# Optimization experiments

Hardware: AMD Instinct MI355X
Metric: run time of the kernel (lower is better)

The kernel has to match this reference:

```python
import jax, jax.numpy as jnp
import numpy as np

STEP_SIZE = 0.01
ITERATION = 1.0
F_FORCING = 8.0
N_STEPS = int(round(ITERATION / STEP_SIZE))  # 100 fixed RK4 steps

BATCH = 8192
INPUT_SIZE = 784
SYSTEM_COUNT = 1024
OUTPUT_SIZE = 10


def setup_inputs() -> dict:
    key = jax.random.key(0)
    k_x, k_w1, k_b1, k_w2, k_b2 = jax.random.split(key, 5)
    x = jax.random.normal(k_x, (BATCH, INPUT_SIZE), dtype=jnp.float32)
    # nn.Linear-style params (out_features, in_features)
    s1 = 1.0 / np.sqrt(INPUT_SIZE)
    W1 = jax.random.uniform(k_w1, (SYSTEM_COUNT, INPUT_SIZE), jnp.float32, -s1, s1)
    b1 = jax.random.uniform(k_b1, (SYSTEM_COUNT,), jnp.float32, -s1, s1)
    s2 = 1.0 / np.sqrt(SYSTEM_COUNT)
    W2 = jax.random.uniform(k_w2, (OUTPUT_SIZE, SYSTEM_COUNT), jnp.float32, -s2, s2)
    b2 = jax.random.uniform(k_b2, (OUTPUT_SIZE,), jnp.float32, -s2, s2)
    return {"x": x, "W1": W1, "b1": b1, "W2": W2, "b2": b2}


def _lorenz96(x):
    # (roll(x,-1) - roll(x,2)) * roll(x,1) - x + F   along feature dim 1
    return (jnp.roll(x, -1, axis=1) - jnp.roll(x, 2, axis=1)) * jnp.roll(x, 1, axis=1) - x + F_FORCING


def _rk4_integrate(x0):
    h = jnp.float32(STEP_SIZE)

    def step(x, _):
        k1 = _lorenz96(x)
        k2 = _lorenz96(x + 0.5 * h * k1)
        k3 = _lorenz96(x + 0.5 * h * k2)
        k4 = _lorenz96(x + h * k3)
        x_next = x + (h / 6.0) * (k1 + 2.0 * k2 + 2.0 * k3 + k4)
        return x_next, None

    xT, _ = jax.lax.scan(step, x0, None, length=N_STEPS)
    return xT


def reference(x, W1, b1, W2, b2):
    h = x @ W1.T + b1                 # [B, systemCount]
    h = _rk4_integrate(h)             # RK4 over [0, iteration], step 0.01
    logits = h @ W2.T + b2            # [B, output_size]
    return jax.nn.log_softmax(logits, axis=1)
```

## Files before the change

### kernel.cpp

```cpp
#include <hip/hip_runtime.h>
#include <hip/hip_bf16.h>
#include <math.h>

#define BATCH 8192
#define INSZ 784
#define SYS 1024
#define OUTSZ 10
#define NSTEP 100
#define HSTEP 0.01f
#define FFORCE 8.0f
#define KP 800

typedef short short8 __attribute__((ext_vector_type(8)));
typedef float float4v __attribute__((ext_vector_type(4)));
typedef float v2f __attribute__((ext_vector_type(2)));

static __device__ __forceinline__ short f2bf(float x) {
    __hip_bfloat16 b = __float2bfloat16(x);
    return __builtin_bit_cast(short, b);
}
static __device__ __forceinline__ float bf2f(short s) {
    unsigned int u = ((unsigned int)(unsigned short)s) << 16;
    return __builtin_bit_cast(float, u);
}

static __device__ __forceinline__ v2f pkfma(v2f a, v2f b, v2f c) {
    return __builtin_elementwise_fma(a, b, c);
}
static __device__ __forceinline__ v2f mk2(float x, float y) {
    v2f r; r.x = x; r.y = y; return r;
}
static __device__ __forceinline__ v2f sh2(v2f v, int ln) {
    v2f r; r.x = __shfl(v.x, ln); r.y = __shfl(v.y, ln); return r;
}

static __device__ __forceinline__ void gld_lds16(const void* g, void* l) {
    __builtin_amdgcn_global_load_lds(
        (const __attribute__((address_space(1))) unsigned int*)g,
        (__attribute__((address_space(3))) unsigned int*)l, 16, 0, 0);
}

__global__ __launch_bounds__(256) void convert_kernel(
    const float* __restrict__ x, const float* __restrict__ W1,
    short* __restrict__ xh, short* __restrict__ xl,
    short* __restrict__ wh, short* __restrict__ wl)
{
    const int total = (BATCH + SYS) * (KP / 8);
    for (int idx = blockIdx.x * blockDim.x + threadIdx.x; idx < total;
         idx += gridDim.x * blockDim.x) {
        const int row = idx / (KP / 8);
        const int ck  = idx - row * (KP / 8);

        short8 hi, lo;
        if (ck < INSZ / 8) {
            const float* src = (row < BATCH)
                ? (x + (size_t)row * INSZ)
                : (W1 + (size_t)(row - BATCH) * INSZ);
            float4 v0 = ((const float4*)src)[ck * 2];
            float4 v1 = ((const float4*)src)[ck * 2 + 1];
            float vv[8] = {v0.x, v0.y, v0.z, v0.w, v1.x, v1.y, v1.z, v1.w};
            #pragma unroll
            for (int j = 0; j < 8; ++j) {
                short hj = f2bf(vv[j]);
                hi[j] = hj;
                lo[j] = f2bf(vv[j] - bf2f(hj));
            }
        } else {
            #pragma unroll
            for (int j = 0; j < 8; ++j) { hi[j] = 0; lo[j] = 0; }
        }

        short* dh; short* dl;
        if (row < BATCH) {
            dh = xh + (size_t)row * KP;
            dl = xl + (size_t)row * KP;
        } else {
            dh = wh + (size_t)(row - BATCH) * KP;
            dl = wl + (size_t)(row - BATCH) * KP;
        }
        *(short8*)(dh + ck * 8) = hi;
        *(short8*)(dl + ck * 8) = lo;
    }
}

#define BM4 128
#define BN4 256
#define BK4 32

__global__ __launch_bounds__(512, 4) void gemm1s_kernel(
    const short* __restrict__ xh, const short* __restrict__ xl,
    const short* __restrict__ wh, const short* __restrict__ wl,
    const float* __restrict__ b1, float* __restrict__ h)
{
    __shared__ short Ah[BM4 * BK4], Al[BM4 * BK4];
    __shared__ short Bh[BN4 * BK4], Bl[BN4 * BK4];

    const int t = threadIdx.x;

    const int lin = blockIdx.y * gridDim.x + blockIdx.x;
    const int cpx = (gridDim.x * gridDim.y) >> 3;
    const int swz = (lin & 7) * cpx + (lin >> 3);
    const int bm  = (swz >> 2) * BM4;
    const int bn  = (swz & 3) * BN4;

    const int wv   = t >> 6;
    const int lane = t & 63;
    const int lm   = lane & 15;
    const int q    = lane >> 4;
    const int wr   = wv >> 2;
    const int wc   = wv & 3;

    float4v acc[4][4];
    #pragma unroll
    for (int mi = 0; mi < 4; ++mi)
        #pragma unroll
        for (int nj = 0; nj < 4; ++nj) {
            acc[mi][nj][0] = 0.f; acc[mi][nj][1] = 0.f;
            acc[mi][nj][2] = 0.f; acc[mi][nj][3] = 0.f;
        }

    const int srA = wv * 16 + (lane >> 2);
    const int kqq = (lane & 3) * 8;
    const short* gAh = xh + (size_t)(bm + srA) * KP + kqq;
    const short* gAl = xl + (size_t)(bm + srA) * KP + kqq;
    const short* gB0h = wh + (size_t)(bn + srA) * KP + kqq;
    const short* gB0l = wl + (size_t)(bn + srA) * KP + kqq;
    const short* gB1h = wh + (size_t)(bn + 128 + srA) * KP + kqq;
    const short* gB1l = wl + (size_t)(bn + 128 + srA) * KP + kqq;

    short* lAh = &Ah[wv * 512];
    short* lAl = &Al[wv * 512];
    short* lB0h = &Bh[wv * 512];
    short* lB0l = &Bl[wv * 512];
    short* lB1h = &Bh[4096 + wv * 512];
    short* lB1l = &Bl[4096 + wv * 512];

    gld_lds16(gAh, lAh);   gld_lds16(gAl, lAl);
    gld_lds16(gB0h, lB0h); gld_lds16(gB0l, lB0l);
    gld_lds16(gB1h, lB1h); gld_lds16(gB1l, lB1l);

    for (int it = 0; it < 25; ++it) {
        __syncthreads();

        short8 fah[4], fal[4];
        #pragma unroll
        for (int mi = 0; mi < 4; ++mi) {
            const int ao = (wr * 64 + mi * 16 + lm) * BK4 + q * 8;
            fah[mi] = *(const short8*)&Ah[ao];
            fal[mi] = *(const short8*)&Al[ao];
        }
        short8 fbh[4], fbl[4];
        #pragma unroll
        for (int nj = 0; nj < 4; ++nj) {
            const int bo = (wc * 64 + nj * 16 + lm) * BK4 + q * 8;
            fbh[nj] = *(const short8*)&Bh[bo];
            fbl[nj] = *(const short8*)&Bl[bo];
        }
        __syncthreads();

        if (it < 24) {
            const int k1 = (it + 1) * BK4;
            gld_lds16(gAh + k1, lAh);   gld_lds16(gAl + k1, lAl);
            gld_lds16(gB0h + k1, lB0h); gld_lds16(gB0l + k1, lB0l);
            gld_lds16(gB1h + k1, lB1h); gld_lds16(gB1l + k1, lB1l);
        }

        #pragma unroll
        for (int nj = 0; nj < 4; ++nj) {
            #pragma unroll
            for (int mi = 0; mi < 4; ++mi) {
                acc[mi][nj] = __builtin_amdgcn_mfma_f32_16x16x32_bf16(fah[mi], fbh[nj], acc[mi][nj], 0, 0, 0);
                acc[mi][nj] = __builtin_amdgcn_mfma_f32_16x16x32_bf16(fah[mi], fbl[nj], acc[mi][nj], 0, 0, 0);
                acc[mi][nj] = __builtin_amdgcn_mfma_f32_16x16x32_bf16(fal[mi], fbh[nj], acc[mi][nj], 0, 0, 0);
            }
        }
    }

    #pragma unroll
    for (int mi = 0; mi < 4; ++mi) {
        const int row0 = bm + wr * 64 + mi * 16 + q * 4;
        #pragma unroll
        for (int nj = 0; nj < 4; ++nj) {
            const int col  = bn + wc * 64 + nj * 16 + lm;
            const float bias = b1[col];
            #pragma unroll
            for (int r = 0; r < 4; ++r)
                h[(size_t)(row0 + r) * SYS + col] = acc[mi][nj][r] + bias;
        }
    }
}

#define BM2 64
#define BN2 64
#define BK2 32
#define LDK2 40

__global__ __launch_bounds__(256, 4) void gemm1_kernel(
    const float* __restrict__ x, const float* __restrict__ W1,
    const float* __restrict__ b1, float* __restrict__ h)
{
    __shared__ short Ah[BM2 * LDK2], Al[BM2 * LDK2];
    __shared__ short Bh[BN2 * LDK2], Bl[BN2 * LDK2];

    const int t  = threadIdx.x;
    const int bm = blockIdx.y * BM2;
    const int bn = blockIdx.x * BN2;

    const int srow = t >> 2;
    const int kq   = (t & 3) * 8;

    const int wv   = t >> 6;
    const int lane = t & 63;
    const int lm   = lane & 15;
    const int q    = lane >> 4;

    float4v acc[4];
    #pragma unroll
    for (int j = 0; j < 4; ++j) {
        acc[j][0] = 0.f; acc[j][1] = 0.f; acc[j][2] = 0.f; acc[j][3] = 0.f;
    }

    const float* xa0 = x  + (size_t)(bm + srow) * INSZ + kq;
    const float* wb0 = W1 + (size_t)(bn + srow) * INSZ + kq;

    for (int it = 0; it < 25; ++it) {
        const int k0 = it * BK2;
        {
            const bool valid = (k0 + kq) < INSZ;
            float va[8], vb[8];
            if (valid) {
                #pragma unroll
                for (int p = 0; p < 2; ++p) {
                    float4 xv = ((const float4*)(xa0 + k0))[p];
                    float4 bv = ((const float4*)(wb0 + k0))[p];
                    va[4*p+0] = xv.x; va[4*p+1] = xv.y; va[4*p+2] = xv.z; va[4*p+3] = xv.w;
                    vb[4*p+0] = bv.x; vb[4*p+1] = bv.y; vb[4*p+2] = bv.z; vb[4*p+3] = bv.w;
                }
            } else {
                #pragma unroll
                for (int j = 0; j < 8; ++j) { va[j] = 0.f; vb[j] = 0.f; }
            }
            short8 ahi, alo, bhi, blo;
            #pragma unroll
            for (int j = 0; j < 8; ++j) {
                short h1 = f2bf(va[j]);
                short l1 = f2bf(va[j] - bf2f(h1));
                short h2 = f2bf(vb[j]);
                short l2 = f2bf(vb[j] - bf2f(h2));
                ahi[j] = h1;  alo[j] = l1;
                bhi[j] = h2;  blo[j] = l2;
            }
            const int base = srow * LDK2 + kq;
            *(short8*)&Ah[base] = ahi;
            *(short8*)&Al[base] = alo;
            *(short8*)&Bh[base] = bhi;
            *(short8*)&Bl[base] = blo;
        }
        __syncthreads();

        const int aoff = (wv * 16 + lm) * LDK2 + q * 8;
        short8 ah = *(const short8*)&Ah[aoff];
        short8 al = *(const short8*)&Al[aoff];
        #pragma unroll
        for (int fj = 0; fj < 4; ++fj) {
            const int boff = (fj * 16 + lm) * LDK2 + q * 8;
            short8 bh = *(const short8*)&Bh[boff];
            short8 bl = *(const short8*)&Bl[boff];
            acc[fj] = __builtin_amdgcn_mfma_f32_16x16x32_bf16(ah, bh, acc[fj], 0, 0, 0);
            acc[fj] = __builtin_amdgcn_mfma_f32_16x16x32_bf16(ah, bl, acc[fj], 0, 0, 0);
            acc[fj] = __builtin_amdgcn_mfma_f32_16x16x32_bf16(al, bh, acc[fj], 0, 0, 0);
        }
        __syncthreads();
    }

    #pragma unroll
    for (int fj = 0; fj < 4; ++fj) {
        const int col  = bn + fj * 16 + lm;
        const float bias = b1[col];
        const int row0 = bm + wv * 16 + q * 4;
        #pragma unroll
        for (int r = 0; r < 4; ++r)
            h[(size_t)(row0 + r) * SYS + col] = acc[fj][r] + bias;
    }
}

__global__ __launch_bounds__(256, 4) void rk4_kernel(
    const float* __restrict__ hbuf, const float* __restrict__ W2,
    const float* __restrict__ b2, float* __restrict__ out)
{
    const int lane = threadIdx.x & 63;
    const int w    = threadIdx.x >> 6;
    const int rowA = blockIdx.x * 8 + w * 2;
    const int rowB = rowA + 1;

    const int laneL = (lane + 63) & 63;
    const int laneR = (lane + 1) & 63;

    v2f X[16];
    {
        const float4* a4 = (const float4*)(hbuf + (size_t)rowA * SYS) + lane * 4;
        const float4* b4 = (const float4*)(hbuf + (size_t)rowB * SYS) + lane * 4;
        #pragma unroll
        for (int k = 0; k < 4; ++k) {
            float4 av = a4[k], bv = b4[k];
            X[4*k+0] = mk2(av.x, bv.x);
            X[4*k+1] = mk2(av.y, bv.y);
            X[4*k+2] = mk2(av.z, bv.z);
            X[4*k+3] = mk2(av.w, bv.w);
        }
    }

    const v2f Fv     = mk2(FFORCE, FFORCE);
    const v2f c_half = mk2(0.5f * HSTEP, 0.5f * HSTEP);
    const v2f c_full = mk2(HSTEP, HSTEP);
    const v2f c_two  = mk2(2.0f, 2.0f);
    const v2f c_six  = mk2(HSTEP / 6.0f, HSTEP / 6.0f);

    v2f acc[16], T[16];

    auto deriv_ip = [&](v2f (&y)[16], v2f r1, v2f l1, v2f l2) {
        v2f y0o = y[0], y1o = y[1], y2o = y[2];
        v2f d0 = Fv - y[0], d1 = Fv - y[1], d15 = Fv - y[15];
        v2f p2 = y0o, p1 = y1o, cur = y[2];
        #pragma unroll
        for (int i = 2; i < 15; ++i) {
            v2f yp1 = (i < 14) ? y[i + 1] : y[15];
            v2f nv  = pkfma(yp1 - p2, p1, Fv - cur);
            p2 = p1; p1 = cur;
            if (i < 14) cur = y[i + 1];
            y[i] = nv;
        }
        y[15] = pkfma(r1 - p2, p1, d15);
        y[1]  = pkfma(y2o - l1, y0o, d1);
        y[0]  = pkfma(y1o - l2, l1, d0);
    };

    v2f r1x = sh2(X[0],  laneR);
    v2f l1x = sh2(X[15], laneL);
    v2f l2x = sh2(X[14], laneL);

    #pragma unroll 1
    for (int s = 0; s < NSTEP; ++s) {
        #pragma unroll
        for (int i = 2; i < 15; ++i)
            acc[i] = pkfma(X[i + 1] - X[i - 2], X[i - 1], Fv - X[i]);
        acc[15] = pkfma(r1x - X[13], X[14], Fv - X[15]);
        acc[1]  = pkfma(X[2] - l1x, X[0],  Fv - X[1]);
        acc[0]  = pkfma(X[1] - l2x, l1x,   Fv - X[0]);

        T[14] = pkfma(c_half, acc[14], X[14]);
        T[15] = pkfma(c_half, acc[15], X[15]);
        T[0]  = pkfma(c_half, acc[0],  X[0]);
        v2f r1 = sh2(T[0],  laneR);
        v2f l1 = sh2(T[15], laneL);
        v2f l2 = sh2(T[14], laneL);
        #pragma unroll
        for (int i = 1; i < 14; ++i) T[i] = pkfma(c_half, acc[i], X[i]);
        deriv_ip(T, r1, l1, l2);

        {
            v2f a;
            a = T[14]; acc[14] = pkfma(c_two, a, acc[14]); T[14] = pkfma(c_half, a, X[14]);
            a = T[15]; acc[15] = pkfma(c_two, a, acc[15]); T[15] = pkfma(c_half, a, X[15]);
            a = T[0];  acc[0]  = pkfma(c_two, a, acc[0]);  T[0]  = pkfma(c_half, a, X[0]);
            r1 = sh2(T[0],  laneR);
            l1 = sh2(T[15], laneL);
            l2 = sh2(T[14], laneL);
            #pragma unroll
            for (int i = 1; i < 14; ++i) {
                a = T[i]; acc[i] = pkfma(c_two, a, acc[i]); T[i] = pkfma(c_half, a, X[i]);
            }
        }
        deriv_ip(T, r1, l1, l2);

        {
            v2f a;
            a = T[14]; acc[14] = pkfma(c_two, a, acc[14]); T[14] = pkfma(c_full, a, X[14]);
            a = T[15]; acc[15] = pkfma(c_two, a, acc[15]); T[15] = pkfma(c_full, a, X[15]);
            a = T[0];  acc[0]  = pkfma(c_two, a, acc[0]);  T[0]  = pkfma(c_full, a, X[0]);
            r1 = sh2(T[0],  laneR);
            l1 = sh2(T[15], laneL);
            l2 = sh2(T[14], laneL);
            #pragma unroll
            for (int i = 1; i < 14; ++i) {
                a = T[i]; acc[i] = pkfma(c_two, a, acc[i]); T[i] = pkfma(c_full, a, X[i]);
            }
        }
        deriv_ip(T, r1, l1, l2);

        X[14] = pkfma(c_six, acc[14] + T[14], X[14]);
        X[15] = pkfma(c_six, acc[15] + T[15], X[15]);
        X[0]  = pkfma(c_six, acc[0]  + T[0],  X[0]);
        r1x = sh2(X[0],  laneR);
        l1x = sh2(X[15], laneL);
        l2x = sh2(X[14], laneL);
        #pragma unroll
        for (int i = 1; i < 14; ++i)
            X[i] = pkfma(c_six, acc[i] + T[i], X[i]);
    }

    v2f l[OUTSZ];
    #pragma unroll
    for (int o = 0; o < OUTSZ; ++o) {
        const float4* w4 = (const float4*)(W2 + (size_t)o * SYS) + lane * 4;
        v2f s2 = mk2(0.f, 0.f);
        #pragma unroll
        for (int k = 0; k < 4; ++k) {
            float4 wv = w4[k];
            s2 = pkfma(X[4*k+0], mk2(wv.x, wv.x), s2);
            s2 = pkfma(X[4*k+1], mk2(wv.y, wv.y), s2);
            s2 = pkfma(X[4*k+2], mk2(wv.z, wv.z), s2);
            s2 = pkfma(X[4*k+3], mk2(wv.w, wv.w), s2);
        }
        #pragma unroll
        for (int dlt = 1; dlt < 64; dlt <<= 1) {
            s2.x += __shfl_xor(s2.x, dlt);
            s2.y += __shfl_xor(s2.y, dlt);
        }
        const float bo = b2[o];
        l[o] = s2 + mk2(bo, bo);
    }

    v2f m = l[0];
    #pragma unroll
    for (int o = 1; o < OUTSZ; ++o) m = __builtin_elementwise_max(m, l[o]);
    v2f ssum = mk2(0.f, 0.f);
    #pragma unroll
    for (int o = 0; o < OUTSZ; ++o) {
        v2f d = l[o] - m;
        ssum = ssum + mk2(__expf(d.x), __expf(d.y));
    }
    const v2f lse = m + mk2(__logf(ssum.x), __logf(ssum.y));

    float vA = l[0].x - lse.x;
    float vB = l[0].y - lse.y;
    #pragma unroll
    for (int o = 1; o < OUTSZ; ++o) {
        if (lane == o) { vA = l[o].x - lse.x; vB = l[o].y - lse.y; }
    }
    if (lane < OUTSZ) {
        out[(size_t)rowA * OUTSZ + lane] = vA;
        out[(size_t)rowB * OUTSZ + lane] = vB;
    }
}

extern "C" void kernel_launch(void* const* d_in, const int* in_sizes, int n_in,
                              void* d_out, int out_size, void* d_ws, size_t ws_size,
                              hipStream_t stream)
{
    const float* x  = (const float*)d_in[0];
    const float* W1 = (const float*)d_in[1];
    const float* b1 = (const float*)d_in[2];
    const float* W2 = (const float*)d_in[3];
    const float* b2 = (const float*)d_in[4];
    float* out = (float*)d_out;
    float* h   = (float*)d_ws;

    const size_t hbytes      = (size_t)BATCH * SYS * sizeof(float);
    const size_t splitshorts = (size_t)(BATCH + SYS) * KP;
    const size_t need        = hbytes + 2 * splitshorts * sizeof(short);

    if (ws_size >= need) {
        short* xh = (short*)((char*)d_ws + hbytes);
        short* xl = xh + (size_t)BATCH * KP;
        short* wh = xl + (size_t)BATCH * KP;
        short* wl = wh + (size_t)SYS * KP;
        convert_kernel<<<2048, 256, 0, stream>>>(x, W1, xh, xl, wh, wl);
        dim3 g1(SYS / BN4, BATCH / BM4);
        gemm1s_kernel<<<g1, 512, 0, stream>>>(xh, xl, wh, wl, b1, h);
    } else {
        dim3 g1(SYS / BN2, BATCH / BM2);
        gemm1_kernel<<<g1, 256, 0, stream>>>(x, W1, b1, h);
    }

    rk4_kernel<<<BATCH / 8, 256, 0, stream>>>(h, W2, b2, out);
}
```

Baseline: 414.3 us.

## Double-buffer LDS tiles in split-bf16 GEMM1 to drop one barrier per K-step

```diff
diff --git a/kernel.cpp b/kernel.cpp
--- a/kernel.cpp
+++ b/kernel.cpp
@@ -92,8 +92,8 @@
     const short* __restrict__ wh, const short* __restrict__ wl,
     const float* __restrict__ b1, float* __restrict__ h)
 {
-    __shared__ short Ah[BM4 * BK4], Al[BM4 * BK4];
-    __shared__ short Bh[BN4 * BK4], Bl[BN4 * BK4];
+    __shared__ short Ah[2][BM4 * BK4], Al[2][BM4 * BK4];
+    __shared__ short Bh[2][BN4 * BK4], Bl[2][BN4 * BK4];
 
     const int t = threadIdx.x;
 
@@ -128,41 +128,39 @@
     const short* gB1h = wh + (size_t)(bn + 128 + srA) * KP + kqq;
     const short* gB1l = wl + (size_t)(bn + 128 + srA) * KP + kqq;
 
-    short* lAh = &Ah[wv * 512];
-    short* lAl = &Al[wv * 512];
-    short* lB0h = &Bh[wv * 512];
-    short* lB0l = &Bl[wv * 512];
-    short* lB1h = &Bh[4096 + wv * 512];
-    short* lB1l = &Bl[4096 + wv * 512];
-
-    gld_lds16(gAh, lAh);   gld_lds16(gAl, lAl);
-    gld_lds16(gB0h, lB0h); gld_lds16(gB0l, lB0l);
-    gld_lds16(gB1h, lB1h); gld_lds16(gB1l, lB1l);
+    gld_lds16(gAh,  &Ah[0][wv * 512]);  gld_lds16(gAl,  &Al[0][wv * 512]);
+    gld_lds16(gB0h, &Bh[0][wv * 512]);  gld_lds16(gB0l, &Bl[0][wv * 512]);
+    gld_lds16(gB1h, &Bh[0][4096 + wv * 512]);
+    gld_lds16(gB1l, &Bl[0][4096 + wv * 512]);
 
     for (int it = 0; it < 25; ++it) {
+        const int p = it & 1;
         __syncthreads();
+
+        if (it < 24) {
+            const int k1 = (it + 1) * BK4;
+            const int n = p ^ 1;
+            gld_lds16(gAh + k1,  &Ah[n][wv * 512]);
+            gld_lds16(gAl + k1,  &Al[n][wv * 512]);
+            gld_lds16(gB0h + k1, &Bh[n][wv * 512]);
+            gld_lds16(gB0l + k1, &Bl[n][wv * 512]);
+            gld_lds16(gB1h + k1, &Bh[n][4096 + wv * 512]);
+            gld_lds16(gB1l + k1, &Bl[n][4096 + wv * 512]);
+        }
 
         short8 fah[4], fal[4];
         #pragma unroll
         for (int mi = 0; mi < 4; ++mi) {
             const int ao = (wr * 64 + mi * 16 + lm) * BK4 + q * 8;
-            fah[mi] = *(const short8*)&Ah[ao];
-            fal[mi] = *(const short8*)&Al[ao];
+            fah[mi] = *(const short8*)&Ah[p][ao];
+            fal[mi] = *(const short8*)&Al[p][ao];
         }
         short8 fbh[4], fbl[4];
         #pragma unroll
         for (int nj = 0; nj < 4; ++nj) {
             const int bo = (wc * 64 + nj * 16 + lm) * BK4 + q * 8;
-            fbh[nj] = *(const short8*)&Bh[bo];
-            fbl[nj] = *(const short8*)&Bl[bo];
-        }
-        __syncthreads();
-
-        if (it < 24) {
-            const int k1 = (it + 1) * BK4;
-            gld_lds16(gAh + k1, lAh);   gld_lds16(gAl + k1, lAl);
-            gld_lds16(gB0h + k1, lB0h); gld_lds16(gB0l + k1, lB0l);
-            gld_lds16(gB1h + k1, lB1h); gld_lds16(gB1l + k1, lB1l);
+            fbh[nj] = *(const short8*)&Bh[p][bo];
+            fbl[nj] = *(const short8*)&Bl[p][bo];
         }
 
         #pragma unroll
```

After: 432.9 us. +4.5%, slower.
